# Kernel tuning notes

Measured on AMD Instinct MI355X. Metric: run time of the kernel, lower is better.

Reference implementation:

```python
import jax, jax.numpy as jnp
import numpy as np

N, D, H, W = 2, 16, 32, 32
C, G, K = 64, 4, 3
PAD, STRIDE, DIL = 1, 1, 1
OS = 1.0
GC = C // G
P = K * K * K
EPS = 1e-6


def setup_inputs() -> dict:
    key = jax.random.key(0)
    ks = jax.random.split(key, 8)
    s = 1.0 / np.sqrt(C)
    return {
        "input": jax.random.normal(ks[0], (N, D, H, W, C), jnp.float32),
        "dw_w": jax.random.normal(ks[1], (C, 1, K, K, K), jnp.float32) * 0.05,
        "dw_b": jnp.zeros((C,), jnp.float32),
        "ln_g": jnp.ones((C,), jnp.float32),
        "ln_b": jnp.zeros((C,), jnp.float32),
        "off_w": jax.random.normal(ks[2], (G * P * 3, C), jnp.float32) * 0.02,
        "off_b": jax.random.normal(ks[3], (G * P * 3,), jnp.float32) * 0.1,
        "mask_w": jax.random.normal(ks[4], (G * P, C), jnp.float32) * 0.02,
        "mask_b": jnp.zeros((G * P,), jnp.float32),
        "in_w": jax.random.normal(ks[5], (C, C), jnp.float32) * s,
        "in_b": jnp.zeros((C,), jnp.float32),
        "out_w": jax.random.normal(ks[6], (C, C), jnp.float32) * s,
        "out_b": jnp.zeros((C,), jnp.float32),
    }


def _grid_sample_3d(inp, grid):
    # inp: (B, Cc, Dd, Hh, Ww); grid: (B, L, Pp, 3) with (x, y, z) in [-1, 1]
    # trilinear, padding_mode='zeros', align_corners=False (torch F.grid_sample semantics)
    B, Cc, Dd, Hh, Ww = inp.shape
    L, Pp = grid.shape[1], grid.shape[2]
    px = ((grid[..., 0] + 1.0) * Ww - 1.0) * 0.5
    py = ((grid[..., 1] + 1.0) * Hh - 1.0) * 0.5
    pz = ((grid[..., 2] + 1.0) * Dd - 1.0) * 0.5
    x0 = jnp.floor(px).astype(jnp.int32)
    y0 = jnp.floor(py).astype(jnp.int32)
    z0 = jnp.floor(pz).astype(jnp.int32)
    fx = px - x0
    fy = py - y0
    fz = pz - z0
    flat = inp.reshape(B, Cc, Dd * Hh * Ww)

    def gather(zi, yi, xi, wt):
        valid = (xi >= 0) & (xi < Ww) & (yi >= 0) & (yi < Hh) & (zi >= 0) & (zi < Dd)
        idx = (jnp.clip(zi, 0, Dd - 1) * Hh + jnp.clip(yi, 0, Hh - 1)) * Ww + jnp.clip(xi, 0, Ww - 1)
        g = jax.vmap(lambda f, i: f[:, i])(flat, idx.reshape(B, -1))  # (B, Cc, L*Pp)
        w = (wt * valid.astype(wt.dtype)).reshape(B, 1, -1)
        return g * w

    out = gather(z0, y0, x0, (1 - fz) * (1 - fy) * (1 - fx))
    out = out + gather(z0, y0, x0 + 1, (1 - fz) * (1 - fy) * fx)
    out = out + gather(z0, y0 + 1, x0, (1 - fz) * fy * (1 - fx))
    out = out + gather(z0, y0 + 1, x0 + 1, (1 - fz) * fy * fx)
    out = out + gather(z0 + 1, y0, x0, fz * (1 - fy) * (1 - fx))
    out = out + gather(z0 + 1, y0, x0 + 1, fz * (1 - fy) * fx)
    out = out + gather(z0 + 1, y0 + 1, x0, fz * fy * (1 - fx))
    out = out + gather(z0 + 1, y0 + 1, x0 + 1, fz * fy * fx)
    return out.reshape(B, Cc, L, Pp)


def _forward(input, dw_w, dw_b, ln_g, ln_b, off_w, off_b, mask_w, mask_b, in_w, in_b, out_w, out_b):
    N_, D_, H_, W_, C_ = input.shape
    # input projection (value path)
    x = input @ in_w.T + in_b
    # depthwise conv -> LayerNorm (channels_last) -> GELU  (the x1 / query path)
    xc = jnp.transpose(input, (0, 4, 1, 2, 3))
    pad = (DIL * 0 + (K - 1)) // 2  # dw_kernel_size == kernel_size, 'same' padding
    y = jax.lax.conv_general_dilated(
        xc, dw_w, window_strides=(1, 1, 1), padding=[(pad, pad)] * 3,
        dimension_numbers=("NCDHW", "OIDHW", "NCDHW"), feature_group_count=C_)
    y = y + dw_b[None, :, None, None, None]
    x1 = jnp.transpose(y, (0, 2, 3, 4, 1))
    mu = x1.mean(-1, keepdims=True)
    var = x1.var(-1, keepdims=True)
    x1 = (x1 - mu) * jax.lax.rsqrt(var + EPS) * ln_g + ln_b
    x1 = jax.nn.gelu(x1, approximate=False)
    # offset and mask heads
    offset = x1 @ off_w.T + off_b                       # (N, D, H, W, G*P*3)
    mlog = (x1 @ mask_w.T + mask_b).reshape(N_, D_, H_, W_, G, P)
    mask = jax.nn.softmax(mlog, axis=-1).reshape(N_, D_, H_, W_, G * P)
    # ---- dcnv3 core ----
    xp = jnp.pad(x, ((0, 0), (PAD, PAD), (PAD, PAD), (PAD, PAD), (0, 0)))
    Din, Hin, Win = D_ + 2 * PAD, H_ + 2 * PAD, W_ + 2 * PAD
    Dout = (Din - (DIL * (K - 1) + 1)) // STRIDE + 1
    Hout = (Hin - (DIL * (K - 1) + 1)) // STRIDE + 1
    Wout = (Win - (DIL * (K - 1) + 1)) // STRIDE + 1
    base = DIL * (K - 1) // 2 + 0.5
    rz = (base + jnp.arange(Dout, dtype=jnp.float32) * STRIDE) / Din
    ry = (base + jnp.arange(Hout, dtype=jnp.float32) * STRIDE) / Hin
    rx = (base + jnp.arange(Wout, dtype=jnp.float32) * STRIDE) / Win
    Z, Y, X = jnp.meshgrid(rz, ry, rx, indexing="ij")
    ref = jnp.stack([X, Y, Z], -1)                       # (Dout, Hout, Wout, 3) in (x,y,z)
    # dilation kernel grid; torch iterates (kw, kh, kd) with 'ij' meshgrid
    off1 = jnp.arange(K, dtype=jnp.float32) * DIL - (DIL * (K - 1) // 2)
    gx, gy, gz = jnp.meshgrid(off1 / Win, off1 / Hin, off1 / Din, indexing="ij")
    gridk = jnp.stack([gx, gy, gz], -1).reshape(P, 3)    # (P, 3), same for every group
    loc = ref[None, :, :, :, None, None, :] + OS * gridk[None, None, None, None, None, :, :]
    offs = offset.reshape(N_, Dout, Hout, Wout, G, P, 3)
    norm = jnp.array([Win, Hin, Din], jnp.float32)
    loc = loc + offs * OS / norm                         # (N, Dout, Hout, Wout, G, P, 3)
    sg = 2.0 * loc - 1.0
    L = Dout * Hout * Wout
    x_ = xp.reshape(N_, Din, Hin, Win, G, GC)
    x_ = jnp.transpose(x_, (0, 4, 5, 1, 2, 3)).reshape(N_ * G, GC, Din, Hin, Win)
    grid_ = sg.reshape(N_, L, G, P, 3)
    grid_ = jnp.transpose(grid_, (0, 2, 1, 3, 4)).reshape(N_ * G, L, P, 3)
    samp = _grid_sample_3d(x_, grid_)                    # (N*G, GC, L, P)
    m_ = jnp.transpose(mask.reshape(N_, L, G, P), (0, 2, 1, 3)).reshape(N_ * G, 1, L, P)
    out = (samp * m_).sum(-1)                            # (N*G, GC, L)
    out = jnp.transpose(out.reshape(N_, G * GC, L), (0, 2, 1)).reshape(N_, Dout, Hout, Wout, C_)
    return out @ out_w.T + out_b


def reference(input, dw_w, dw_b, ln_g, ln_b, off_w, off_b, mask_w, mask_b, in_w, in_b, out_w, out_b):
    return _forward(input, dw_w, dw_b, ln_g, ln_b, off_w, off_b, mask_w, mask_b, in_w, in_b, out_w, out_b)
```

## Files before the change

### kernel.cpp

```cpp
#include <hip/hip_runtime.h>
#include <math.h>


#define NN 2
#define DD 16
#define HH 32
#define WW 32
#define DIN 18
#define HIN 34
#define WIN 34
#define NVOX 32768
#define NPAD (NN*DIN*HIN*WIN)
#define PLANE (DIN*HIN*WIN)
#define ROWS 432
#define SOMSTR 436

#define WS_XPG     16
#define XPG_FLOATS (NPAD*32)
#define WS_DWT     (WS_XPG + XPG_FLOATS + 16)
#define WS_CMBB    (WS_DWT + 1728)
#define WS_OUTB    (WS_CMBB + 13824)
#define WS_INB     (WS_OUTB + 2048)
#define ZERO_F4    ((16 + XPG_FLOATS + 16) / 4)

typedef short  bf16x8 __attribute__((ext_vector_type(8)));
typedef float  f32x4  __attribute__((ext_vector_type(4)));

__device__ __forceinline__ unsigned short f2bf(float x) {
    unsigned u = __builtin_bit_cast(unsigned, x);
    u += 0x7fff + ((u >> 16) & 1);
    return (unsigned short)(u >> 16);
}
__device__ __forceinline__ float bf2f(unsigned short v) {
    return __builtin_bit_cast(float, ((unsigned)v) << 16);
}
__device__ __forceinline__ float bflo(unsigned u) {
    return __builtin_bit_cast(float, u << 16);
}
__device__ __forceinline__ float bfhi(unsigned u) {
    return __builtin_bit_cast(float, u & 0xffff0000u);
}
__device__ __forceinline__ bf16x8 pack8(float4 a, float4 b) {
    bf16x8 r;
    r[0] = (short)f2bf(a.x); r[1] = (short)f2bf(a.y);
    r[2] = (short)f2bf(a.z); r[3] = (short)f2bf(a.w);
    r[4] = (short)f2bf(b.x); r[5] = (short)f2bf(b.y);
    r[6] = (short)f2bf(b.z); r[7] = (short)f2bf(b.w);
    return r;
}

__global__ __launch_bounds__(256) void setup(
        const float* __restrict__ in_w,  const float* __restrict__ out_w,
        const float* __restrict__ off_w, const float* __restrict__ mask_w,
        const float* __restrict__ dw_w,  float* __restrict__ ws) {
    int t = blockIdx.x * 256 + threadIdx.x;
    if (t < ZERO_F4)
        ((float4*)ws)[t] = make_float4(0.f, 0.f, 0.f, 0.f);
    if (t < 1728) {
        int k = t >> 6, c = t & 63;
        ws[WS_DWT + t] = dw_w[c * 27 + k];
    }
    if (t < 27648) {
        unsigned short* cmbB = (unsigned short*)(ws + WS_CMBB);
        cmbB[t] = f2bf(t < 20736 ? off_w[t] : mask_w[t - 20736]);
    }
    if (t < 4096) {
        ((unsigned short*)(ws + WS_OUTB))[t] = f2bf(out_w[t]);
        ((unsigned short*)(ws + WS_INB))[t]  = f2bf(in_w[t]);
    }
}

__global__ __launch_bounds__(256) void value_proj(
        const float* __restrict__ inp,
        const float* __restrict__ ws_ro,
        const float* __restrict__ in_b,
        float* __restrict__ ws_out) {
    const unsigned short* inB = (const unsigned short*)(ws_ro + WS_INB);
    unsigned short* xpg = (unsigned short*)(ws_out + WS_XPG);
    int hw = blockIdx.x;
    int L = (hw & 7) * 64 + (hw >> 3);
    int u = threadIdx.x >> 6, lane = threadIdx.x & 63;
    int nid = lane & 15, quad = lane >> 4;
    int v0 = L * 64 + u * 16;

    int vx = v0 + nid;
    int w = vx & 31, h = (vx >> 5) & 31, d = (vx >> 10) & 15, n = vx >> 14;
    int pvox = ((n * DIN + d + 1) * HIN + h + 1) * WIN + (w + 1);

    const float* ip = inp + (size_t)vx * 64;
    bf16x8 b0 = pack8(*(const float4*)(ip + quad * 8),
                      *(const float4*)(ip + quad * 8 + 4));
    bf16x8 b1 = pack8(*(const float4*)(ip + quad * 8 + 32),
                      *(const float4*)(ip + quad * 8 + 36));

    #pragma unroll
    for (int t = 0; t < 4; ++t) {
        bf16x8 a0 = *(const bf16x8*)&inB[(16 * t + nid) * 64 + quad * 8];
        bf16x8 a1 = *(const bf16x8*)&inB[(16 * t + nid) * 64 + quad * 8 + 32];
        f32x4 acc = {0.f, 0.f, 0.f, 0.f};
        acc = __builtin_amdgcn_mfma_f32_16x16x32_bf16(a0, b0, acc, 0, 0, 0);
        acc = __builtin_amdgcn_mfma_f32_16x16x32_bf16(a1, b1, acc, 0, 0, 0);
        float bs0 = in_b[16 * t + 4 * quad + 0];
        float bs1 = in_b[16 * t + 4 * quad + 1];
        float bs2 = in_b[16 * t + 4 * quad + 2];
        float bs3 = in_b[16 * t + 4 * quad + 3];
        unsigned d0 = (unsigned)f2bf(acc[0] + bs0) | ((unsigned)f2bf(acc[1] + bs1) << 16);
        unsigned d1 = (unsigned)f2bf(acc[2] + bs2) | ((unsigned)f2bf(acc[3] + bs3) << 16);
        *(uint2*)&xpg[((size_t)t * NPAD + pvox) * 16 + 4 * quad] = make_uint2(d0, d1);
    }
}

__global__ __launch_bounds__(256, 6) void dcn_main(
        const float* __restrict__ inp,
        const float* __restrict__ dw_b,
        const float* __restrict__ ln_g,  const float* __restrict__ ln_b,
        const float* __restrict__ off_b, const float* __restrict__ mask_b,
        const float* __restrict__ ws_ro,
        const float* __restrict__ out_b,
        float* __restrict__ out) {
    const unsigned short* xpg  = (const unsigned short*)(ws_ro + WS_XPG);
    const float* dwT  = ws_ro + WS_DWT;
    const unsigned short* cmbB = (const unsigned short*)(ws_ro + WS_CMBB);
    const unsigned short* outB = (const unsigned short*)(ws_ro + WS_OUTB);

    __shared__ __align__(16) unsigned short s_a[16 * 64];
    __shared__ unsigned short s_om[16 * SOMSTR];
    __shared__ __align__(16) unsigned short s_vb[16 * 64];

    int t = threadIdx.x;
    int u = t >> 6, lane = t & 63;
    int nid = lane & 15, quad = lane >> 4;
    int hw = blockIdx.x;
    int L = (hw & 7) * 256 + (hw >> 3);
    int vox0 = L * 16;
    int w0 = vox0 & 31;
    int h0 = (vox0 >> 5) & 31;
    int d0 = (vox0 >> 10) & 15;
    int n  = vox0 >> 14;

    {
        int c = lane;
        float dwb = dw_b[c];
        float acc[4] = {dwb, dwb, dwb, dwb};
        int wbase = w0 + u * 4;
        #pragma unroll
        for (int kd = 0; kd < 3; ++kd) {
            int dz = d0 + kd - 1;
            if ((unsigned)dz >= DD) continue;
            #pragma unroll
            for (int kh = 0; kh < 3; ++kh) {
                int hy = h0 + kh - 1;
                if ((unsigned)hy >= HH) continue;
                const float* rowp = inp + ((((size_t)n * DD + dz) * HH + hy) * WW) * 64 + c;
                float cv[6];
                #pragma unroll
                for (int j = 0; j < 6; ++j) {
                    int wx = wbase - 1 + j;
                    cv[j] = ((unsigned)wx < WW) ? rowp[(size_t)wx * 64] : 0.f;
                }
                float wt0 = dwT[(kd * 9 + kh * 3 + 0) * 64 + c];
                float wt1 = dwT[(kd * 9 + kh * 3 + 1) * 64 + c];
                float wt2 = dwT[(kd * 9 + kh * 3 + 2) * 64 + c];
                #pragma unroll
                for (int i = 0; i < 4; ++i) {
                    acc[i] = fmaf(cv[i],     wt0, acc[i]);
                    acc[i] = fmaf(cv[i + 1], wt1, acc[i]);
                    acc[i] = fmaf(cv[i + 2], wt2, acc[i]);
                }
            }
        }
        #pragma unroll
        for (int i = 0; i < 4; ++i) {
            float a = acc[i];
            float s = a, ss = a * a;
            #pragma unroll
            for (int m = 1; m < 64; m <<= 1) {
                s  += __shfl_xor(s,  m, 64);
                ss += __shfl_xor(ss, m, 64);
            }
            float mu  = s * (1.f / 64.f);
            float var = ss * (1.f / 64.f) - mu * mu;
            float x1 = (a - mu) * rsqrtf(var + 1e-6f) * ln_g[c] + ln_b[c];
            x1 = 0.5f * x1 * (1.f + erff(x1 * 0.70710678118654752f));
            s_a[(u * 4 + i) * 64 + c] = f2bf(x1);
        }
    }
    __syncthreads();

    {
        bf16x8 a0 = *(const bf16x8*)&s_a[nid * 64 + quad * 8];
        bf16x8 a1 = *(const bf16x8*)&s_a[nid * 64 + quad * 8 + 32];
        for (int tl = u; tl < 27; tl += 4) {
            int r = tl * 16 + nid;
            bf16x8 b0 = *(const bf16x8*)&cmbB[r * 64 + quad * 8];
            bf16x8 b1 = *(const bf16x8*)&cmbB[r * 64 + quad * 8 + 32];
            f32x4 acc = {0.f, 0.f, 0.f, 0.f};
            acc = __builtin_amdgcn_mfma_f32_16x16x32_bf16(a0, b0, acc, 0, 0, 0);
            acc = __builtin_amdgcn_mfma_f32_16x16x32_bf16(a1, b1, acc, 0, 0, 0);
            float bias = (r < 324) ? off_b[r] : mask_b[r - 324];
            #pragma unroll
            for (int k = 0; k < 4; ++k)
                s_om[(quad * 4 + k) * SOMSTR + r] = f2bf(acc[k] + bias);
        }
    }
    __syncthreads();

    {
        int pair = t >> 2, l = t & 3;
        int vb = pair >> 2, g = pair & 3;
        unsigned short* m = &s_om[vb * SOMSTR + 324 + g * 27];
        float e[7];
        float mx = -1e30f;
        #pragma unroll
        for (int j = 0; j < 7; ++j) {
            int p = l + 4 * j;
            float v = (p < 27) ? bf2f(m[p]) : -1e30f;
            e[j] = v;
            mx = fmaxf(mx, v);
        }
        mx = fmaxf(mx, __shfl_xor(mx, 1, 64));
        mx = fmaxf(mx, __shfl_xor(mx, 2, 64));
        float sm = 0.f;
        #pragma unroll
        for (int j = 0; j < 7; ++j) {
            int p = l + 4 * j;
            e[j] = (p < 27) ? expf(e[j] - mx) : 0.f;
            sm += e[j];
        }
        sm += __shfl_xor(sm, 1, 64);
        sm += __shfl_xor(sm, 2, 64);
        float inv = 1.f / sm;
        #pragma unroll
        for (int j = 0; j < 7; ++j) {
            int p = l + 4 * j;
            if (p < 27) m[p] = f2bf(e[j] * inv);
        }
    }
    __syncthreads();

    {
        int vb = lane >> 2, q = lane & 3;
        int chalf = q & 1, xhalf = q >> 1;
        int qo = q * 8;
        int wv = w0 + vb;
        const unsigned short* om = &s_om[vb * SOMSTR];
        const unsigned short* xg = xpg + ((size_t)u * NPAD + (size_t)n * PLANE) * 16;
        float acc[8] = {0.f, 0.f, 0.f, 0.f, 0.f, 0.f, 0.f, 0.f};
        int p = 0;
        #pragma unroll
        for (int ix = 0; ix < 3; ++ix)
        #pragma unroll
        for (int iy = 0; iy < 3; ++iy)
        #pragma unroll
        for (int iz = 0; iz < 3; ++iz, ++p) {
            int rb = (u * 27 + p) * 3;
            float ox = bf2f(om[rb + 0]), oy = bf2f(om[rb + 1]), oz = bf2f(om[rb + 2]);
            float msk = bf2f(om[324 + u * 27 + p]);
            float px = (float)(wv + ix) + ox;
            float py = (float)(h0 + iy) + oy;
            float pz = (float)(d0 + iz) + oz;
            float fx0 = floorf(px); int x0 = (int)fx0; float fx = px - fx0;
            float fy0 = floorf(py); int y0 = (int)fy0; float fy = py - fy0;
            float fz0 = floorf(pz); int z0 = (int)fz0; float fz = pz - fz0;
            float wx0 = ((unsigned)x0       < WIN) ? (1.f - fx) : 0.f;
            float wx1 = ((unsigned)(x0 + 1) < WIN) ? fx         : 0.f;
            float wy0 = ((unsigned)y0       < HIN) ? (1.f - fy) : 0.f;
            float wy1 = ((unsigned)(y0 + 1) < HIN) ? fy         : 0.f;
            float wz0 = ((unsigned)z0       < DIN) ? (1.f - fz) : 0.f;
            float wz1 = ((unsigned)(z0 + 1) < DIN) ? fz         : 0.f;
            wz0 *= msk; wz1 *= msk;
            int x0c = min(max(x0, -1), WIN - 1);
            int y0c = min(max(y0, 0), HIN - 1), y1c = min(max(y0 + 1, 0), HIN - 1);
            int z0c = min(max(z0, 0), DIN - 1), z1c = min(max(z0 + 1, 0), DIN - 1);
            int r00 = (z0c * HIN + y0c) * WIN + x0c;
            int r01 = (z0c * HIN + y1c) * WIN + x0c;
            int r10 = (z1c * HIN + y0c) * WIN + x0c;
            int r11 = (z1c * HIN + y1c) * WIN + x0c;
            uint4 t00 = *(const uint4*)(xg + r00 * 16 + qo);
            uint4 t01 = *(const uint4*)(xg + r01 * 16 + qo);
            uint4 t10 = *(const uint4*)(xg + r10 * 16 + qo);
            uint4 t11 = *(const uint4*)(xg + r11 * 16 + qo);
            float wxq = xhalf ? wx1 : wx0;
            float w00 = wxq * wz0 * wy0;
            float w01 = wxq * wz0 * wy1;
            float w10 = wxq * wz1 * wy0;
            float w11 = wxq * wz1 * wy1;
            #define ACC8(T, W) { float w_ = (W); \
                acc[0] = fmaf(w_, bflo(T.x), acc[0]); acc[1] = fmaf(w_, bfhi(T.x), acc[1]); \
                acc[2] = fmaf(w_, bflo(T.y), acc[2]); acc[3] = fmaf(w_, bfhi(T.y), acc[3]); \
                acc[4] = fmaf(w_, bflo(T.z), acc[4]); acc[5] = fmaf(w_, bfhi(T.z), acc[5]); \
                acc[6] = fmaf(w_, bflo(T.w), acc[6]); acc[7] = fmaf(w_, bfhi(T.w), acc[7]); }
            ACC8(t00, w00) ACC8(t01, w01) ACC8(t10, w10) ACC8(t11, w11)
            #undef ACC8
        }
        #pragma unroll
        for (int i = 0; i < 8; ++i) acc[i] += __shfl_xor(acc[i], 2, 64);
        if (q < 2) {
            unsigned d0 = (unsigned)f2bf(acc[0]) | ((unsigned)f2bf(acc[1]) << 16);
            unsigned d1 = (unsigned)f2bf(acc[2]) | ((unsigned)f2bf(acc[3]) << 16);
            unsigned d2 = (unsigned)f2bf(acc[4]) | ((unsigned)f2bf(acc[5]) << 16);
            unsigned d3 = (unsigned)f2bf(acc[6]) | ((unsigned)f2bf(acc[7]) << 16);
            *(uint4*)&s_vb[vb * 64 + u * 16 + chalf * 8] = make_uint4(d0, d1, d2, d3);
        }
    }
    __syncthreads();

    {
        bf16x8 a0 = *(const bf16x8*)&s_vb[nid * 64 + quad * 8];
        bf16x8 a1 = *(const bf16x8*)&s_vb[nid * 64 + quad * 8 + 32];
        bf16x8 b0 = *(const bf16x8*)&outB[(u * 16 + nid) * 64 + quad * 8];
        bf16x8 b1 = *(const bf16x8*)&outB[(u * 16 + nid) * 64 + quad * 8 + 32];
        f32x4 acc = {0.f, 0.f, 0.f, 0.f};
        acc = __builtin_amdgcn_mfma_f32_16x16x32_bf16(a0, b0, acc, 0, 0, 0);
        acc = __builtin_amdgcn_mfma_f32_16x16x32_bf16(a1, b1, acc, 0, 0, 0);
        float ob = out_b[u * 16 + nid];
        #pragma unroll
        for (int k = 0; k < 4; ++k)
            out[(size_t)(vox0 + quad * 4 + k) * 64 + u * 16 + nid] = acc[k] + ob;
    }
}

extern "C" void kernel_launch(void* const* d_in, const int* in_sizes, int n_in,
                              void* d_out, int out_size, void* d_ws, size_t ws_size,
                              hipStream_t stream) {
    const float* inp    = (const float*)d_in[0];
    const float* dw_w   = (const float*)d_in[1];
    const float* dw_b   = (const float*)d_in[2];
    const float* ln_g   = (const float*)d_in[3];
    const float* ln_b   = (const float*)d_in[4];
    const float* off_w  = (const float*)d_in[5];
    const float* off_b  = (const float*)d_in[6];
    const float* mask_w = (const float*)d_in[7];
    const float* mask_b = (const float*)d_in[8];
    const float* in_w   = (const float*)d_in[9];
    const float* in_b   = (const float*)d_in[10];
    const float* out_w  = (const float*)d_in[11];
    const float* out_b  = (const float*)d_in[12];

    float* ws = (float*)d_ws;

    setup<<<1302, 256, 0, stream>>>(in_w, out_w, off_w, mask_w, dw_w, ws);
    value_proj<<<NVOX / 64, 256, 0, stream>>>(inp, ws, in_b, ws);
    dcn_main<<<NVOX / 16, 256, 0, stream>>>(inp, dw_b, ln_g, ln_b,
                                            off_b, mask_b, ws, out_b,
                                            (float*)d_out);
}
```

Measured before the change: 155.7 us.

## Fuse weight prep with value projection and interleave offset/mask records in LDS

Merges the setup and value_proj kernels into one prep_vp kernel. It launches one block per 16 padded voxels and writes zeros directly for halo voxels, so the separate full-buffer zeroing pass over the padded value tensor goes away. Each block converts in_w to bf16 in shared memory, and all four waves compute the same 16 voxels, so some work is repeated. In dcn_main, the three offsets and the mask for each sample point are now stored as one 4-element record in LDS and read with a single 8-byte load. Trilinear address arithmetic is also lightly restructured.

Result: no change. 158.4 us (+1.8%).

```diff
diff --git a/kernel.cpp b/kernel.cpp
--- a/kernel.cpp
+++ b/kernel.cpp
@@ -1,6 +1,5 @@
 #include <hip/hip_runtime.h>
 #include <math.h>
-
 
 #define NN 2
 #define DD 16
@@ -20,8 +19,13 @@
 #define WS_DWT     (WS_XPG + XPG_FLOATS + 16)
 #define WS_CMBB    (WS_DWT + 1728)
 #define WS_OUTB    (WS_CMBB + 13824)
-#define WS_INB     (WS_OUTB + 2048)
-#define ZERO_F4    ((16 + XPG_FLOATS + 16) / 4)
+
+#define PREP_DWT   1728
+#define PREP_CMB   27648
+#define PREP_OUT   4096
+#define PREP_PADS  32
+#define PREP_TOTAL (PREP_DWT + PREP_CMB + PREP_OUT + PREP_PADS)
+#define PREP_BLOCKS 131
 
 typedef short  bf16x8 __attribute__((ext_vector_type(8)));
 typedef float  f32x4  __attribute__((ext_vector_type(4)));
@@ -49,64 +53,74 @@
     return r;
 }
 
-__global__ __launch_bounds__(256) void setup(
+__global__ __launch_bounds__(256) void prep_vp(
+        const float* __restrict__ inp,
         const float* __restrict__ in_w,  const float* __restrict__ out_w,
         const float* __restrict__ off_w, const float* __restrict__ mask_w,
-        const float* __restrict__ dw_w,  float* __restrict__ ws) {
-    int t = blockIdx.x * 256 + threadIdx.x;
-    if (t < ZERO_F4)
-        ((float4*)ws)[t] = make_float4(0.f, 0.f, 0.f, 0.f);
-    if (t < 1728) {
-        int k = t >> 6, c = t & 63;
-        ws[WS_DWT + t] = dw_w[c * 27 + k];
-    }
-    if (t < 27648) {
-        unsigned short* cmbB = (unsigned short*)(ws + WS_CMBB);
-        cmbB[t] = f2bf(t < 20736 ? off_w[t] : mask_w[t - 20736]);
-    }
-    if (t < 4096) {
-        ((unsigned short*)(ws + WS_OUTB))[t] = f2bf(out_w[t]);
-        ((unsigned short*)(ws + WS_INB))[t]  = f2bf(in_w[t]);
-    }
-}
-
-__global__ __launch_bounds__(256) void value_proj(
-        const float* __restrict__ inp,
-        const float* __restrict__ ws_ro,
-        const float* __restrict__ in_b,
-        float* __restrict__ ws_out) {
-    const unsigned short* inB = (const unsigned short*)(ws_ro + WS_INB);
-    unsigned short* xpg = (unsigned short*)(ws_out + WS_XPG);
-    int hw = blockIdx.x;
-    int L = (hw & 7) * 64 + (hw >> 3);
-    int u = threadIdx.x >> 6, lane = threadIdx.x & 63;
+        const float* __restrict__ dw_w,  const float* __restrict__ in_b,
+        float* __restrict__ ws) {
+    __shared__ __align__(16) unsigned short inB[4096];
+
+    int t = threadIdx.x;
+    int b = blockIdx.x;
+
+    for (int i = t; i < 4096; i += 256) inB[i] = f2bf(in_w[i]);
+
+    if (b < PREP_BLOCKS) {
+        int idx = b * 256 + t;
+        if (idx < PREP_DWT) {
+            int k = idx >> 6, c = idx & 63;
+            ws[WS_DWT + idx] = dw_w[c * 27 + k];
+        } else if (idx < PREP_DWT + PREP_CMB) {
+            int j = idx - PREP_DWT;
+            ((unsigned short*)(ws + WS_CMBB))[j] =
+                f2bf(j < 20736 ? off_w[j] : mask_w[j - 20736]);
+        } else if (idx < PREP_DWT + PREP_CMB + PREP_OUT) {
+            int j = idx - PREP_DWT - PREP_CMB;
+            ((unsigned short*)(ws + WS_OUTB))[j] = f2bf(out_w[j]);
+        } else if (idx < PREP_TOTAL) {
+            int j = idx - PREP_DWT - PREP_CMB - PREP_OUT;
+            if (j < 16) ws[j] = 0.f;
+            else        ws[WS_XPG + XPG_FLOATS + (j - 16)] = 0.f;
+        }
+    }
+    __syncthreads();
+
+    unsigned short* xpg = (unsigned short*)(ws + WS_XPG);
+    int lane = t & 63;
     int nid = lane & 15, quad = lane >> 4;
-    int v0 = L * 64 + u * 16;
-
-    int vx = v0 + nid;
-    int w = vx & 31, h = (vx >> 5) & 31, d = (vx >> 10) & 15, n = vx >> 14;
-    int pvox = ((n * DIN + d + 1) * HIN + h + 1) * WIN + (w + 1);
-
-    const float* ip = inp + (size_t)vx * 64;
-    bf16x8 b0 = pack8(*(const float4*)(ip + quad * 8),
-                      *(const float4*)(ip + quad * 8 + 4));
-    bf16x8 b1 = pack8(*(const float4*)(ip + quad * 8 + 32),
-                      *(const float4*)(ip + quad * 8 + 36));
+
+    int pv = b * 16 + nid;
+    int wp = pv % 34, hp = (pv / 34) % 34, dp = (pv / 1156) % 18, n = pv / 20808;
+    bool interior = (wp >= 1 && wp <= 32 && hp >= 1 && hp <= 32 && dp >= 1 && dp <= 16);
+
+    bf16x8 b0 = {0,0,0,0,0,0,0,0}, b1 = {0,0,0,0,0,0,0,0};
+    if (interior) {
+        int vox = (((n * 16 + (dp - 1)) * 32 + (hp - 1)) * 32) + (wp - 1);
+        const float* ip = inp + (size_t)vox * 64;
+        b0 = pack8(*(const float4*)(ip + quad * 8),
+                   *(const float4*)(ip + quad * 8 + 4));
+        b1 = pack8(*(const float4*)(ip + quad * 8 + 32),
+                   *(const float4*)(ip + quad * 8 + 36));
+    }
 
     #pragma unroll
-    for (int t = 0; t < 4; ++t) {
-        bf16x8 a0 = *(const bf16x8*)&inB[(16 * t + nid) * 64 + quad * 8];
-        bf16x8 a1 = *(const bf16x8*)&inB[(16 * t + nid) * 64 + quad * 8 + 32];
+    for (int tt = 0; tt < 4; ++tt) {
+        bf16x8 a0 = *(const bf16x8*)&inB[(16 * tt + nid) * 64 + quad * 8];
+        bf16x8 a1 = *(const bf16x8*)&inB[(16 * tt + nid) * 64 + quad * 8 + 32];
         f32x4 acc = {0.f, 0.f, 0.f, 0.f};
         acc = __builtin_amdgcn_mfma_f32_16x16x32_bf16(a0, b0, acc, 0, 0, 0);
         acc = __builtin_amdgcn_mfma_f32_16x16x32_bf16(a1, b1, acc, 0, 0, 0);
-        float bs0 = in_b[16 * t + 4 * quad + 0];
-        float bs1 = in_b[16 * t + 4 * quad + 1];
-        float bs2 = in_b[16 * t + 4 * quad + 2];
-        float bs3 = in_b[16 * t + 4 * quad + 3];
-        unsigned d0 = (unsigned)f2bf(acc[0] + bs0) | ((unsigned)f2bf(acc[1] + bs1) << 16);
-        unsigned d1 = (unsigned)f2bf(acc[2] + bs2) | ((unsigned)f2bf(acc[3] + bs3) << 16);
-        *(uint2*)&xpg[((size_t)t * NPAD + pvox) * 16 + 4 * quad] = make_uint2(d0, d1);
+        float bs0 = in_b[16 * tt + 4 * quad + 0];
+        float bs1 = in_b[16 * tt + 4 * quad + 1];
+        float bs2 = in_b[16 * tt + 4 * quad + 2];
+        float bs3 = in_b[16 * tt + 4 * quad + 3];
+        unsigned d0 = 0u, d1 = 0u;
+        if (interior) {
+            d0 = (unsigned)f2bf(acc[0] + bs0) | ((unsigned)f2bf(acc[1] + bs1) << 16);
+            d1 = (unsigned)f2bf(acc[2] + bs2) | ((unsigned)f2bf(acc[3] + bs3) << 16);
+        }
+        *(uint2*)&xpg[((size_t)tt * NPAD + pv) * 16 + 4 * quad] = make_uint2(d0, d1);
     }
 }
 
@@ -124,7 +138,7 @@
     const unsigned short* outB = (const unsigned short*)(ws_ro + WS_OUTB);
 
     __shared__ __align__(16) unsigned short s_a[16 * 64];
-    __shared__ unsigned short s_om[16 * SOMSTR];
+    __shared__ __align__(16) unsigned short s_om2[16 * SOMSTR];
     __shared__ __align__(16) unsigned short s_vb[16 * 64];
 
     int t = threadIdx.x;
@@ -197,10 +211,18 @@
             f32x4 acc = {0.f, 0.f, 0.f, 0.f};
             acc = __builtin_amdgcn_mfma_f32_16x16x32_bf16(a0, b0, acc, 0, 0, 0);
             acc = __builtin_amdgcn_mfma_f32_16x16x32_bf16(a1, b1, acc, 0, 0, 0);
-            float bias = (r < 324) ? off_b[r] : mask_b[r - 324];
+            float bias;
+            int addr;
+            if (r < 324) {
+                bias = off_b[r];
+                addr = (r / 3) * 4 + (r % 3);
+            } else {
+                bias = mask_b[r - 324];
+                addr = (r - 324) * 4 + 3;
+            }
             #pragma unroll
             for (int k = 0; k < 4; ++k)
-                s_om[(quad * 4 + k) * SOMSTR + r] = f2bf(acc[k] + bias);
+                s_om2[(quad * 4 + k) * SOMSTR + addr] = f2bf(acc[k] + bias);
         }
     }
     __syncthreads();
@@ -208,13 +230,13 @@
     {
         int pair = t >> 2, l = t & 3;
         int vb = pair >> 2, g = pair & 3;
-        unsigned short* m = &s_om[vb * SOMSTR + 324 + g * 27];
+        unsigned short* m = &s_om2[vb * SOMSTR + g * 108];
         float e[7];
         float mx = -1e30f;
         #pragma unroll
         for (int j = 0; j < 7; ++j) {
             int p = l + 4 * j;
-            float v = (p < 27) ? bf2f(m[p]) : -1e30f;
+            float v = (p < 27) ? bf2f(m[p * 4 + 3]) : -1e30f;
             e[j] = v;
             mx = fmaxf(mx, v);
         }
@@ -233,7 +255,7 @@
         #pragma unroll
         for (int j = 0; j < 7; ++j) {
             int p = l + 4 * j;
-            if (p < 27) m[p] = f2bf(e[j] * inv);
+            if (p < 27) m[p * 4 + 3] = f2bf(e[j] * inv);
         }
     }
     __syncthreads();
@@ -243,7 +265,7 @@
         int chalf = q & 1, xhalf = q >> 1;
         int qo = q * 8;
         int wv = w0 + vb;
-        const unsigned short* om = &s_om[vb * SOMSTR];
+        const unsigned short* omb = &s_om2[vb * SOMSTR + u * 108];
         const unsigned short* xg = xpg + ((size_t)u * NPAD + (size_t)n * PLANE) * 16;
         float acc[8] = {0.f, 0.f, 0.f, 0.f, 0.f, 0.f, 0.f, 0.f};
         int p = 0;
@@ -253,9 +275,9 @@
         for (int iy = 0; iy < 3; ++iy)
         #pragma unroll
         for (int iz = 0; iz < 3; ++iz, ++p) {
-            int rb = (u * 27 + p) * 3;
-            float ox = bf2f(om[rb + 0]), oy = bf2f(om[rb + 1]), oz = bf2f(om[rb + 2]);
-            float msk = bf2f(om[324 + u * 27 + p]);
+            uint2 om4 = *(const uint2*)&omb[p * 4];
+            float ox = bflo(om4.x), oy = bfhi(om4.x);
+            float oz = bflo(om4.y), msk = bfhi(om4.y);
             float px = (float)(wv + ix) + ox;
             float py = (float)(h0 + iy) + oy;
             float pz = (float)(d0 + iz) + oz;
@@ -272,10 +294,12 @@
             int x0c = min(max(x0, -1), WIN - 1);
             int y0c = min(max(y0, 0), HIN - 1), y1c = min(max(y0 + 1, 0), HIN - 1);
             int z0c = min(max(z0, 0), DIN - 1), z1c = min(max(z0 + 1, 0), DIN - 1);
-            int r00 = (z0c * HIN + y0c) * WIN + x0c;
-            int r01 = (z0c * HIN + y1c) * WIN + x0c;
-            int r10 = (z1c * HIN + y0c) * WIN + x0c;
-            int r11 = (z1c * HIN + y1c) * WIN + x0c;
+            int zb0 = z0c * (HIN * WIN), zb1 = z1c * (HIN * WIN);
+            int yb0 = y0c * WIN,         yb1 = y1c * WIN;
+            int r00 = zb0 + yb0 + x0c;
+            int r01 = zb0 + yb1 + x0c;
+            int r10 = zb1 + yb0 + x0c;
+            int r11 = zb1 + yb1 + x0c;
             uint4 t00 = *(const uint4*)(xg + r00 * 16 + qo);
             uint4 t01 = *(const uint4*)(xg + r01 * 16 + qo);
             uint4 t10 = *(const uint4*)(xg + r10 * 16 + qo);
@@ -339,8 +363,8 @@
 
     float* ws = (float*)d_ws;
 
-    setup<<<1302, 256, 0, stream>>>(in_w, out_w, off_w, mask_w, dw_w, ws);
-    value_proj<<<NVOX / 64, 256, 0, stream>>>(inp, ws, in_b, ws);
+    prep_vp<<<NPAD / 16, 256, 0, stream>>>(inp, in_w, out_w, off_w, mask_w,
+                                           dw_w, in_b, ws);
     dcn_main<<<NVOX / 16, 256, 0, stream>>>(inp, dw_b, ln_g, ln_b,
                                             off_b, mask_b, ws, out_b,
                                             (float*)d_out);
```
